# Kernel optimization log

Hardware: AMD Instinct MI355X
Metric: run time of the kernel (lower is better)

## Reference

```python
import jax, jax.numpy as jnp
import numpy as np
from jax import lax

B, C, F, T = 32, 1, 128, 8000
FLOOR = 1e-06


def setup_inputs() -> dict:
    key = jax.random.key(0)
    mag_spec = jax.random.uniform(key, (B, C, F, T), dtype=jnp.float32)  # non-negative magnitudes
    alpha = jnp.full((C,), 0.96, dtype=jnp.float32)
    delta = jnp.full((C,), 2.0, dtype=jnp.float32)
    root = jnp.full((C,), 2.0, dtype=jnp.float32)
    smooth = jnp.full((1,), 0.04, dtype=jnp.float32)  # per_channel_smoothing=False -> shape (1,)
    return {"mag_spec": mag_spec, "alpha": alpha, "delta": delta, "root": root, "smooth": smooth}


def reference(mag_spec, alpha, delta, root, smooth):
    # mag_spec: [B, C, F, T]
    w = jnp.clip(smooth, 0.0, 1.0)[:, None]          # broadcast over (C, F) per time-step
    xs = jnp.moveaxis(mag_spec, -1, 0)               # [T, B, C, F]
    init = xs[0]                                     # initial_state = mag_spec[..., 0]

    def step(acc, x):
        acc = w * x + (1.0 - w) * acc
        return acc, acc

    final, ema = lax.scan(step, init, xs)            # ema: [T, B, C, F]
    ema = jnp.moveaxis(ema, 0, -1)                   # [B, C, F, T]

    a = jnp.minimum(alpha, 1.0)[:, None, None]       # (C,1,1) -> broadcast over F,T
    d = delta[:, None, None]
    one_over_root = 1.0 / jnp.maximum(root, 1.0)[:, None, None]

    out = (mag_spec / (FLOOR + ema) ** a + d) ** one_over_root - d ** one_over_root
    hidden_state = final[..., None]                  # [B, C, F, 1]
    return out, hidden_state
```

## Files before the change

### kernel.cpp

```cpp
#include <hip/hip_runtime.h>

#define FLOOR_EPS 1e-6f

constexpr int Bq = 32, Cq = 1, Fq = 128, Tq = 8000;
constexpr int ROWS = Bq * Cq * Fq;
constexpr int LPT  = 32;
constexpr int NTH  = 256;
constexpr int ACTIVE = Tq / LPT;

__global__ __launch_bounds__(NTH)
void _PCEN_75033078661345_kernel(const float* __restrict__ x,
                                 const float* __restrict__ alpha,
                                 const float* __restrict__ delta,
                                 const float* __restrict__ root,
                                 const float* __restrict__ smooth,
                                 float* __restrict__ out,
                                 float* __restrict__ hid)
{
    const int r    = blockIdx.x;
    const int t    = threadIdx.x;
    const int lane = t & 63;
    const int wid  = t >> 6;

    const int c = (r / Fq) % Cq;
    const float w   = fminf(fmaxf(smooth[0], 0.f), 1.f);
    const float om  = 1.f - w;
    const float aa  = fminf(alpha[c], 1.f);
    const float dd  = delta[c];
    const float oor = 1.f / fmaxf(root[c], 1.f);

    const float* row = x + (size_t)r * Tq;

    float xv[LPT];
    float Aa = 1.f, cb = 0.f;
    if (t < ACTIVE) {
        const float4* p = (const float4*)(row + t * LPT);
        #pragma unroll
        for (int j = 0; j < LPT / 4; ++j) {
            float4 v = p[j];
            xv[4*j+0] = v.x; xv[4*j+1] = v.y; xv[4*j+2] = v.z; xv[4*j+3] = v.w;
        }
        float acc = 0.f;
        #pragma unroll
        for (int j = 0; j < LPT; ++j)
            acc = w * xv[j] + om * acc;
        cb = acc;
        float om2 = om * om, om4 = om2 * om2, om8 = om4 * om4, om16 = om8 * om8;
        Aa = om16 * om16;
    }

    float a = Aa, b = cb;
    #pragma unroll
    for (int d = 1; d < 64; d <<= 1) {
        float pa = __shfl_up(a, d);
        float pb = __shfl_up(b, d);
        if (lane >= d) { b = a * pb + b; a = a * pa; }
    }
    float lea = __shfl_up(a, 1);
    float leb = __shfl_up(b, 1);
    if (lane == 0) { lea = 1.f; leb = 0.f; }

    __shared__ float swa[NTH / 64], swb[NTH / 64];
    if (lane == 63) { swa[wid] = a; swb[wid] = b; }
    __syncthreads();
    float wpa = 1.f, wpb = 0.f;
    for (int i = 0; i < wid; ++i) {
        float fa = swa[i], fb = swb[i];
        wpb = fa * wpb + fb;
        wpa = fa * wpa;
    }
    const float Ea = lea * wpa;
    const float Eb = lea * wpb + leb;

    const float x0 = row[0];
    if (t < ACTIVE) {
        float acc = Ea * x0 + Eb;
        const bool  use_sqrt = (oor == 0.5f);
        const float droot = use_sqrt ? __builtin_amdgcn_sqrtf(dd)
                                     : __builtin_amdgcn_exp2f(oor * __builtin_amdgcn_logf(dd));
        float* orow = out + (size_t)r * Tq + t * LPT;
        #pragma unroll
        for (int j = 0; j < LPT / 4; ++j) {
            float4 o;
            float* op = &o.x;
            #pragma unroll
            for (int k = 0; k < 4; ++k) {
                float xx = xv[4*j + k];
                acc = w * xx + om * acc;
                float dp = __builtin_amdgcn_exp2f(-aa * __builtin_amdgcn_logf(FLOOR_EPS + acc));
                float tt = xx * dp + dd;
                float oo = use_sqrt ? (__builtin_amdgcn_sqrtf(tt) - droot)
                                    : (__builtin_amdgcn_exp2f(oor * __builtin_amdgcn_logf(tt)) - droot);
                op[k] = oo;
            }
            ((float4*)orow)[j] = o;
        }
        if (t == ACTIVE - 1)
            hid[r] = acc;
    }
}

extern "C" void kernel_launch(void* const* d_in, const int* in_sizes, int n_in,
                              void* d_out, int out_size, void* d_ws, size_t ws_size,
                              hipStream_t stream) {
    const float* x      = (const float*)d_in[0];
    const float* alpha  = (const float*)d_in[1];
    const float* delta  = (const float*)d_in[2];
    const float* root   = (const float*)d_in[3];
    const float* smooth = (const float*)d_in[4];
    float* out = (float*)d_out;
    float* hid = out + (size_t)ROWS * Tq;

    _PCEN_75033078661345_kernel<<<ROWS, NTH, 0, stream>>>(
        x, alpha, delta, root, smooth, out, hid);
}
```

Baseline: 62.33 us.

## Process each row with one wavefront using chunked scans and prefetching

Each row is now handled by a single 64-lane wavefront instead of a 256-thread block. The wavefront walks the row in rounds of 512 elements, running a wavefront-level scan per round and carrying the EMA state between rounds. A three-slot register buffer prefetches the input two rounds ahead. The aim is to drop the shared-memory/__syncthreads cross-wave combine, stop idling the inactive threads in the last wave (only 250 of 256 were used), and overlap loads with compute. In exchange, each lane serialises 16 rounds, each with shuffle latency, and rows per block are fixed at four.

```diff
diff --git a/kernel.cpp b/kernel.cpp
--- a/kernel.cpp
+++ b/kernel.cpp
@@ -4,11 +4,13 @@
 
 constexpr int Bq = 32, Cq = 1, Fq = 128, Tq = 8000;
 constexpr int ROWS = Bq * Cq * Fq;
-constexpr int LPT  = 32;
-constexpr int NTH  = 256;
-constexpr int ACTIVE = Tq / LPT;
+constexpr int LPR  = 8;
+constexpr int RNDE = 64 * LPR;
+constexpr int NR   = (Tq + RNDE - 1) / RNDE;
+constexpr int LACT = (Tq - (NR - 1) * RNDE) / LPR;
+constexpr int WPB  = 4;
 
-__global__ __launch_bounds__(NTH)
+__global__ __launch_bounds__(256, 4)
 void _PCEN_75033078661345_kernel(const float* __restrict__ x,
                                  const float* __restrict__ alpha,
                                  const float* __restrict__ delta,
@@ -17,87 +19,95 @@
                                  float* __restrict__ out,
                                  float* __restrict__ hid)
 {
-    const int r    = blockIdx.x;
-    const int t    = threadIdx.x;
-    const int lane = t & 63;
-    const int wid  = t >> 6;
+    const int lane = threadIdx.x & 63;
+    const int wid  = threadIdx.x >> 6;
+    const int r    = blockIdx.x * WPB + wid;
+    const int c    = (r / Fq) % Cq;
 
-    const int c = (r / Fq) % Cq;
     const float w   = fminf(fmaxf(smooth[0], 0.f), 1.f);
     const float om  = 1.f - w;
     const float aa  = fminf(alpha[c], 1.f);
     const float dd  = delta[c];
     const float oor = 1.f / fmaxf(root[c], 1.f);
+    const bool  us  = (oor == 0.5f);
+    const float droot = us ? __builtin_amdgcn_sqrtf(dd)
+                           : __builtin_amdgcn_exp2f(oor * __builtin_amdgcn_logf(dd));
 
-    const float* row = x + (size_t)r * Tq;
+    float om2 = om * om, om4 = om2 * om2;
+    float omp[6];
+    omp[0] = om4 * om4;
+    #pragma unroll
+    for (int k = 1; k < 6; ++k) omp[k] = omp[k - 1] * omp[k - 1];
+    float om8i = 1.f;
+    #pragma unroll
+    for (int k = 0; k < 6; ++k) om8i = ((lane >> k) & 1) ? om8i * omp[k] : om8i;
+    const float omR = omp[5] * omp[5];
 
-    float xv[LPT];
-    float Aa = 1.f, cb = 0.f;
-    if (t < ACTIVE) {
-        const float4* p = (const float4*)(row + t * LPT);
-        #pragma unroll
-        for (int j = 0; j < LPT / 4; ++j) {
-            float4 v = p[j];
-            xv[4*j+0] = v.x; xv[4*j+1] = v.y; xv[4*j+2] = v.z; xv[4*j+3] = v.w;
-        }
-        float acc = 0.f;
-        #pragma unroll
-        for (int j = 0; j < LPT; ++j)
-            acc = w * xv[j] + om * acc;
-        cb = acc;
-        float om2 = om * om, om4 = om2 * om2, om8 = om4 * om4, om16 = om8 * om8;
-        Aa = om16 * om16;
+    const float* row  = x   + (size_t)r * Tq;
+    float*       orow = out + (size_t)r * Tq;
+
+    float carry = row[0];
+
+    float4 buf[3][2];
+    #pragma unroll
+    for (int s = 0; s < 2; ++s) {
+        const float4* p = (const float4*)(row + s * RNDE + lane * LPR);
+        buf[s][0] = p[0]; buf[s][1] = p[1];
     }
 
-    float a = Aa, b = cb;
+    float accL = 0.f;
     #pragma unroll
-    for (int d = 1; d < 64; d <<= 1) {
-        float pa = __shfl_up(a, d);
-        float pb = __shfl_up(b, d);
-        if (lane >= d) { b = a * pb + b; a = a * pa; }
+    for (int s = 0; s < NR; ++s) {
+        if (s + 2 < NR) {
+            const bool pact = (s + 2 < NR - 1) || (lane < LACT);
+            float4 n0 = {0,0,0,0}, n1 = {0,0,0,0};
+            if (pact) {
+                const float4* p = (const float4*)(row + (s + 2) * RNDE + lane * LPR);
+                n0 = p[0]; n1 = p[1];
+            }
+            buf[(s + 2) % 3][0] = n0; buf[(s + 2) % 3][1] = n1;
+        }
+
+        const float4 c0 = buf[s % 3][0], c1 = buf[s % 3][1];
+        const float xv[LPR] = {c0.x, c0.y, c0.z, c0.w, c1.x, c1.y, c1.z, c1.w};
+
+        float b = 0.f;
+        #pragma unroll
+        for (int j = 0; j < LPR; ++j) b = w * xv[j] + om * b;
+
+        #pragma unroll
+        for (int k = 0; k < 6; ++k) {
+            const float pb = __shfl_up(b, 1 << k);
+            const float nb = fmaf(omp[k], pb, b);
+            b = (lane >= (1 << k)) ? nb : b;
+        }
+        const float pb1 = __shfl_up(b, 1);
+        const float bex = (lane == 0) ? 0.f : pb1;
+        float acc = fmaf(om8i, carry, bex);
+        const float btot = __shfl(b, 63);
+        carry = fmaf(omR, carry, btot);
+
+        float ov[LPR];
+        #pragma unroll
+        for (int j = 0; j < LPR; ++j) {
+            acc = w * xv[j] + om * acc;
+            const float dp = __builtin_amdgcn_exp2f(-aa * __builtin_amdgcn_logf(FLOOR_EPS + acc));
+            const float tt = fmaf(xv[j], dp, dd);
+            ov[j] = us ? (__builtin_amdgcn_sqrtf(tt) - droot)
+                       : (__builtin_amdgcn_exp2f(oor * __builtin_amdgcn_logf(tt)) - droot);
+        }
+        const bool act = (s < NR - 1) || (lane < LACT);
+        if (act) {
+            float4* q = (float4*)(orow + s * RNDE + lane * LPR);
+            float4 o0 = {ov[0], ov[1], ov[2], ov[3]};
+            float4 o1 = {ov[4], ov[5], ov[6], ov[7]};
+            q[0] = o0; q[1] = o1;
+        }
+        accL = acc;
     }
-    float lea = __shfl_up(a, 1);
-    float leb = __shfl_up(b, 1);
-    if (lane == 0) { lea = 1.f; leb = 0.f; }
 
-    __shared__ float swa[NTH / 64], swb[NTH / 64];
-    if (lane == 63) { swa[wid] = a; swb[wid] = b; }
-    __syncthreads();
-    float wpa = 1.f, wpb = 0.f;
-    for (int i = 0; i < wid; ++i) {
-        float fa = swa[i], fb = swb[i];
-        wpb = fa * wpb + fb;
-        wpa = fa * wpa;
-    }
-    const float Ea = lea * wpa;
-    const float Eb = lea * wpb + leb;
-
-    const float x0 = row[0];
-    if (t < ACTIVE) {
-        float acc = Ea * x0 + Eb;
-        const bool  use_sqrt = (oor == 0.5f);
-        const float droot = use_sqrt ? __builtin_amdgcn_sqrtf(dd)
-                                     : __builtin_amdgcn_exp2f(oor * __builtin_amdgcn_logf(dd));
-        float* orow = out + (size_t)r * Tq + t * LPT;
-        #pragma unroll
-        for (int j = 0; j < LPT / 4; ++j) {
-            float4 o;
-            float* op = &o.x;
-            #pragma unroll
-            for (int k = 0; k < 4; ++k) {
-                float xx = xv[4*j + k];
-                acc = w * xx + om * acc;
-                float dp = __builtin_amdgcn_exp2f(-aa * __builtin_amdgcn_logf(FLOOR_EPS + acc));
-                float tt = xx * dp + dd;
-                float oo = use_sqrt ? (__builtin_amdgcn_sqrtf(tt) - droot)
-                                    : (__builtin_amdgcn_exp2f(oor * __builtin_amdgcn_logf(tt)) - droot);
-                op[k] = oo;
-            }
-            ((float4*)orow)[j] = o;
-        }
-        if (t == ACTIVE - 1)
-            hid[r] = acc;
-    }
+    const float h = __shfl(accL, LACT - 1);
+    if (lane == 0) hid[r] = h;
 }
 
 extern "C" void kernel_launch(void* const* d_in, const int* in_sizes, int n_in,
@@ -111,6 +121,6 @@
     float* out = (float*)d_out;
     float* hid = out + (size_t)ROWS * Tq;
 
-    _PCEN_75033078661345_kernel<<<ROWS, NTH, 0, stream>>>(
+    _PCEN_75033078661345_kernel<<<ROWS / WPB, 256, 0, stream>>>(
         x, alpha, delta, root, smooth, out, hid);
 }
```

Result: no change. 63.09 us (+1.2%).
